# Optimization experiments

Hardware: AMD Instinct MI355X
Metric: run time of the kernel (lower is better)

The kernel has to match this reference:

```python
import jax, jax.numpy as jnp
import numpy as np

B, H, W = 64, 224, 224
EPS = 1e-5


def setup_inputs() -> dict:
    key = jax.random.key(0)
    ks = jax.random.split(key, 8)
    n = lambda k, s, std: jax.random.normal(k, s, jnp.float32) * std
    return {
        "x": jax.random.normal(ks[0], (B, 1, H, W), jnp.float32),
        "conv1_w": n(ks[1], (24, 1, 3, 3), 0.2),
        "conv1_b": jnp.zeros((24,), jnp.float32),
        "bn1_g": jnp.ones((24,), jnp.float32),
        "bn1_b": jnp.zeros((24,), jnp.float32),
        "conv2_w": n(ks[2], (48, 24, 3, 3), 0.07),
        "conv2_b": jnp.zeros((48,), jnp.float32),
        "bn2_g": jnp.ones((48,), jnp.float32),
        "bn2_b": jnp.zeros((48,), jnp.float32),
        "fconv_w": n(ks[3], (48, 48, 56, 56), 0.003),
        "fconv_b": jnp.zeros((48,), jnp.float32),
        "lin1_w": n(ks[4], (24, 48), 0.02),
        "lin1_b": jnp.zeros((24,), jnp.float32),
        "lin2_w": n(ks[5], (4, 24), 0.01),
        "lin2_b": jnp.array([0.0, 0.0, 1.0, 0.0], jnp.float32),  # torch init: identity transform bias
    }


def conv2d(x, w, b):
    y = jax.lax.conv_general_dilated(x, w, (1, 1), ((1, 1), (1, 1)),
                                     dimension_numbers=("NCHW", "OIHW", "NCHW"))
    return y + b[None, :, None, None]


def batchnorm(x, g, b):
    # train-mode BN: batch statistics over (N, H, W), biased variance
    m = x.mean((0, 2, 3), keepdims=True)
    v = x.var((0, 2, 3), keepdims=True)
    return (x - m) * jax.lax.rsqrt(v + EPS) * g[None, :, None, None] + b[None, :, None, None]


def maxpool2(x):
    b, c, h, w = x.shape
    return x.reshape(b, c, h // 2, 2, w // 2, 2).max(axis=(3, 5))


def affine_grid(theta, h, w):
    # theta: [B,2,3]; align_corners=False normalized coords (torch default)
    xs = (jnp.arange(w, dtype=jnp.float32) * 2 + 1) / w - 1.0
    ys = (jnp.arange(h, dtype=jnp.float32) * 2 + 1) / h - 1.0
    gx, gy = jnp.meshgrid(xs, ys)                      # [H,W] each
    base = jnp.stack([gx, gy, jnp.ones_like(gx)], -1)  # [H,W,3] (x, y, 1)
    return jnp.einsum("bij,hwj->bhwi", theta, base)    # [B,H,W,2] -> (x, y)


def grid_sample(img, grid):
    # bilinear, zeros padding, align_corners=False (torch defaults)
    b, c, h, w = img.shape
    ix = ((grid[..., 0] + 1.0) * w - 1.0) * 0.5        # [B,H,W]
    iy = ((grid[..., 1] + 1.0) * h - 1.0) * 0.5
    x0 = jnp.floor(ix); y0 = jnp.floor(iy)
    x1 = x0 + 1.0; y1 = y0 + 1.0
    wx1 = ix - x0; wx0 = 1.0 - wx1
    wy1 = iy - y0; wy0 = 1.0 - wy1
    bidx = jnp.arange(b)[:, None, None]

    def tap(xf, yf, wgt):
        valid = (xf >= 0) & (xf < w) & (yf >= 0) & (yf < h)
        xi = jnp.clip(xf, 0, w - 1).astype(jnp.int32)
        yi = jnp.clip(yf, 0, h - 1).astype(jnp.int32)
        vals = img[bidx, :, yi, xi]                    # [B,H,W,C]
        return vals * (wgt * valid)[..., None]

    out = (tap(x0, y0, wx0 * wy0) + tap(x1, y0, wx1 * wy0)
           + tap(x0, y1, wx0 * wy1) + tap(x1, y1, wx1 * wy1))
    return jnp.transpose(out, (0, 3, 1, 2))            # [B,C,H,W]


def reference(x, conv1_w, conv1_b, bn1_g, bn1_b, conv2_w, conv2_b, bn2_g, bn2_b,
              fconv_w, fconv_b, lin1_w, lin1_b, lin2_w, lin2_b):
    b, _, h, w = x.shape
    x1 = maxpool2(jax.nn.relu(batchnorm(conv2d(x, conv1_w, conv1_b), bn1_g, bn1_b)))
    x1 = maxpool2(jax.nn.relu(batchnorm(conv2d(x1, conv2_w, conv2_b), bn2_g, bn2_b)))
    # final_conv with kernel 56 over a 56x56 map == full contraction
    feat = jnp.einsum("bchw,ochw->bo", x1, fconv_w) + fconv_b      # [B,48]
    theta4 = jax.nn.relu(feat @ lin1_w.T + lin1_b) @ lin2_w.T + lin2_b  # [B,4]
    tx, ty, scale, angle = theta4[:, 0], theta4[:, 1], theta4[:, 2], theta4[:, 3]
    c, s = jnp.cos(angle), jnp.sin(angle)
    # (T @ R @ S)[:, :2] built directly, fully vectorized over batch
    row0 = jnp.stack([scale * c, -scale * s, tx], -1)
    row1 = jnp.stack([scale * s, scale * c, ty], -1)
    theta = jnp.stack([row0, row1], 1)                 # [B,2,3]
    grid = affine_grid(theta, h, w)
    out = grid_sample(x, grid)
    return out, tx, ty, scale, angle
```

## Files before the change

### kernel.cpp

```cpp
#include <hip/hip_runtime.h>
#include <hip/hip_bf16.h>

#define NB 64
#define H0 224
#define W0 224
#define C1 24
#define C2 48
#define H1 112
#define W1 112
#define H2 56
#define W2 56
#define EPSV 1e-5f

#define WS_STATS1   0
#define WS_STATS2   432
#define WS_FEAT     1296
#define WS_B2       4368
#define WS_X2       11280
#define WS_FWT      (WS_X2 + 4818944)
#define WS_X1       9645072
#define WS_NEED_BIG ((size_t)(WS_X1 + 9633792) * 4)
#define OUT0_ELEMS  (NB*H0*W0)

typedef _Float16 v8h __attribute__((ext_vector_type(8)));
typedef float    v4f __attribute__((ext_vector_type(4)));

static __device__ __forceinline__ unsigned short f2h(float v) {
    _Float16 h = (_Float16)v;
    unsigned short us;
    __builtin_memcpy(&us, &h, 2);
    return us;
}

__global__ __launch_bounds__(256) void k_init(const float* __restrict__ w2, float* __restrict__ ws)
{
    int t = blockIdx.x * 256 + threadIdx.x;
    if (t < WS_B2) ws[t] = 0.f;
    if (t < 13824) {
        int e = t & 7;
        int l = (t >> 3) & 63;
        int g = t >> 9;
        int q = l >> 4, ml = l & 15;
        int kp = g / 3, nt = g % 3;
        int ic = q * 8 + e;
        int oc = nt * 16 + ml;
        float v = (ic < C1) ? w2[(oc * C1 + ic) * 9 + kp] : 0.f;
        ((_Float16*)(ws + WS_B2))[t] = (_Float16)v;
    }
}

__global__ __launch_bounds__(256) void k_prep(const float* __restrict__ fw, _Float16* __restrict__ fwt)
{
    int t = blockIdx.x * 256 + threadIdx.x;
    if (t >= 903168) return;
    int o = t / 18816;
    int k = (t % 18816) * 8;
    const float* src = fw + (long)o * 150528 + k;
    float4 v0 = *(const float4*)src;
    float4 v1 = *(const float4*)(src + 4);
    uint4 u;
    u.x = (unsigned int)f2h(v0.x) | ((unsigned int)f2h(v0.y) << 16);
    u.y = (unsigned int)f2h(v0.z) | ((unsigned int)f2h(v0.w) << 16);
    u.z = (unsigned int)f2h(v1.x) | ((unsigned int)f2h(v1.y) << 16);
    u.w = (unsigned int)f2h(v1.z) | ((unsigned int)f2h(v1.w) << 16);
    int g = k >> 6, kin = k & 63;
    *(uint4*)&fwt[((long)(g * 48 + o)) * 64 + kin] = u;
}

__global__ __launch_bounds__(256) void k_conv1_pool_stats4(
    const float* __restrict__ x, const float* __restrict__ w1, const float* __restrict__ b1,
    float* __restrict__ ws, _Float16* __restrict__ x1g)
{
    __shared__ float xt[34][36];
    __shared__ unsigned int outt[256][13];
    __shared__ float sred[2 * C1];

    const int tid = threadIdx.x;
    const int b = blockIdx.z;
    const int py0 = blockIdx.y * 16, px0 = blockIdx.x * 16;
    const int iy0 = 2 * py0 - 1, ix0 = 2 * px0 - 1;
    const float* xb = x + b * (H0 * W0);

    for (int li = tid; li < 34 * 34; li += 256) {
        int ry = li / 34, rx = li % 34;
        int gy = iy0 + ry, gx = ix0 + rx;
        bool ok = (gy >= 0) & (gy < H0) & (gx >= 0) & (gx < W0);
        xt[ry][rx] = ok ? xb[gy * W0 + gx] : 0.f;
    }

    const int wid = tid >> 6;
    const int lane = tid & 63;
    const int c0 = wid * 6;

    const int c0s = __builtin_amdgcn_readfirstlane(c0);
    const float* __restrict__ wps = w1 + c0s * 9;
    float wr[54], br[6];
#pragma unroll
    for (int k = 0; k < 54; k++) wr[k] = wps[k];
#pragma unroll
    for (int c = 0; c < 6; c++) br[c] = b1[c0s + c];

    __syncthreads();

    float s[6] = {0.f, 0.f, 0.f, 0.f, 0.f, 0.f};
    float q[6] = {0.f, 0.f, 0.f, 0.f, 0.f, 0.f};
    const int pc = lane & 15;
    const int pr0 = lane >> 4;

#pragma unroll
    for (int pp = 0; pp < 4; pp++) {
        const int pr = pr0 + 4 * pp;
        float patch[16];
#pragma unroll
        for (int i2 = 0; i2 < 4; i2++)
#pragma unroll
            for (int j2 = 0; j2 < 4; j2++)
                patch[i2 * 4 + j2] = xt[2 * pr + i2][2 * pc + j2];

        unsigned int pk[3];
#pragma unroll
        for (int cp = 0; cp < 3; cp++) {
            unsigned int pv = 0;
#pragma unroll
            for (int h = 0; h < 2; h++) {
                int c = 2 * cp + h;
                float m4 = -1e30f;
#pragma unroll
                for (int sy = 0; sy < 2; sy++)
#pragma unroll
                    for (int sx = 0; sx < 2; sx++) {
                        float a = br[c];
#pragma unroll
                        for (int ky = 0; ky < 3; ky++)
#pragma unroll
                            for (int kx = 0; kx < 3; kx++)
                                a = fmaf(patch[(sy + ky) * 4 + (sx + kx)], wr[c * 9 + ky * 3 + kx], a);
                        s[c] += a;
                        q[c] = fmaf(a, a, q[c]);
                        m4 = fmaxf(m4, a);
                    }
                pv |= ((unsigned int)f2h(m4)) << (16 * h);
            }
            pk[cp] = pv;
        }
        int pos = pr * 16 + pc;
        outt[pos][wid * 3 + 0] = pk[0];
        outt[pos][wid * 3 + 1] = pk[1];
        outt[pos][wid * 3 + 2] = pk[2];
    }

#pragma unroll
    for (int c = 0; c < 6; c++) {
#pragma unroll
        for (int off = 32; off > 0; off >>= 1) {
            s[c] += __shfl_down(s[c], off, 64);
            q[c] += __shfl_down(q[c], off, 64);
        }
    }
    if (lane == 0) {
#pragma unroll
        for (int c = 0; c < 6; c++) {
            sred[c0 + c] = s[c];
            sred[C1 + c0 + c] = q[c];
        }
    }
    __syncthreads();

    if (tid < 2 * C1) {
        int cp = (blockIdx.x + 7 * blockIdx.y + 49 * blockIdx.z) & 7;
        atomicAdd(&ws[WS_STATS1 + cp * 2 * C1 + tid], sred[tid]);
    }

    for (int u = tid; u < 768; u += 256) {
        int pos = u / 3, prt = u % 3;
        int pr = pos >> 4, pcc = pos & 15;
        long p = (long)(b * H1 + (py0 + pr)) * W1 + (px0 + pcc);
        uint4 v;
        v.x = outt[pos][4 * prt + 0];
        v.y = outt[pos][4 * prt + 1];
        v.z = outt[pos][4 * prt + 2];
        v.w = outt[pos][4 * prt + 3];
        *(uint4*)(x1g + p * C1 + prt * 8) = v;
    }
}

__global__ __launch_bounds__(256, 2) void k_conv2_fused5(
    const _Float16* __restrict__ x1g, const _Float16* __restrict__ bpp,
    const float* __restrict__ g1, const float* __restrict__ bb1,
    const float* __restrict__ b2,
    float* __restrict__ ws, unsigned int* __restrict__ pooltu)
{
    __shared__ __align__(16) _Float16 x1t[2][10][18][32];
    __shared__ float alds[C1], bflds[C1];
    __shared__ float sred[2 * C2];

    const int tid = threadIdx.x;
    const int w = tid >> 6;
    const int lane = tid & 63;
    const int ml = lane & 15;
    const int qq = lane >> 4;

    v8h B[9][3];
#pragma unroll
    for (int kp = 0; kp < 9; kp++)
#pragma unroll
        for (int nt = 0; nt < 3; nt++)
            B[kp][nt] = *(const v8h*)&bpp[((kp * 3 + nt) * 64 + lane) * 8];

    if (tid < C1) {
        float s = 0.f, q = 0.f;
#pragma unroll
        for (int i = 0; i < 8; i++) {
            s += ws[WS_STATS1 + i * 2 * C1 + tid];
            q += ws[WS_STATS1 + i * 2 * C1 + C1 + tid];
        }
        const float N = (float)(NB * H0 * W0);
        float m = s / N;
        float v = q / N - m * m;
        float a = g1[tid] / sqrtf(v + EPSV);
        alds[tid] = a;
        bflds[tid] = bb1[tid] - m * a;
    }
    if (tid < 2 * C2) sred[tid] = 0.f;

    float bias[3] = {b2[ml], b2[16 + ml], b2[32 + ml]};

    int spart[3], spr[3], spc[3]; bool swrite[3];
#pragma unroll
    for (int it3 = 0; it3 < 3; it3++) {
        int li = tid + it3 * 256;
        swrite[it3] = li < 720;
        spart[it3] = li & 3;
        int pos = li >> 2;
        spr[it3] = pos / 18;
        spc[it3] = pos % 18;
    }

    const int nb = gridDim.x;
    const int NTILE = 6272;
    int qn = NTILE / nb, rn = NTILE % nb;
    int start = (blockIdx.x < rn) ? blockIdx.x * (qn + 1)
                                  : rn * (qn + 1) + (blockIdx.x - rn) * qn;
    int cnt = (blockIdx.x < rn) ? qn + 1 : qn;

    float svacc[3] = {0.f, 0.f, 0.f}, qvacc[3] = {0.f, 0.f, 0.f};

    v8h raw[3];
    bool inb_n[3];
    {
        int t = start;
        int tb = t / 98, rem = t % 98;
        int ty = (rem / 7) * 8, txx = (rem % 7) * 16;
#pragma unroll
        for (int it3 = 0; it3 < 3; it3++) {
#pragma unroll
            for (int e = 0; e < 8; e++) raw[it3][e] = (_Float16)0.f;
            int gy = ty - 1 + spr[it3], gx = txx - 1 + spc[it3];
            inb_n[it3] = swrite[it3] & (spart[it3] < 3) &
                         (gy >= 0) & (gy < H1) & (gx >= 0) & (gx < W1);
            if (inb_n[it3])
                raw[it3] = *(const v8h*)&x1g[((tb * H1 + gy) * W1 + gx) * C1 + spart[it3] * 8];
        }
    }
    __syncthreads();

#pragma unroll
    for (int it3 = 0; it3 < 3; it3++) {
        if (swrite[it3]) {
            v8h r8;
            if (inb_n[it3]) {
#pragma unroll
                for (int e = 0; e < 8; e++) {
                    int c = spart[it3] * 8 + e;
                    float vv = fmaxf(fmaf((float)raw[it3][e], alds[c], bflds[c]), 0.f);
                    r8[e] = (_Float16)vv;
                }
            } else {
#pragma unroll
                for (int e = 0; e < 8; e++) r8[e] = (_Float16)0.f;
            }
            *(v8h*)&x1t[0][spr[it3]][spc[it3]][spart[it3] * 8] = r8;
        }
    }
    __syncthreads();

    for (int it = 0; it < cnt; it++) {
        const int cur = it & 1;
        const int t = start + it;
        const int tb = t / 98, rem = t % 98;
        const int ty = (rem / 7) * 8, txx = (rem % 7) * 16;

        const bool haveNext = (it + 1 < cnt);
        if (haveNext) {
            int t2 = t + 1;
            int nb2 = t2 / 98, rem2 = t2 % 98;
            int ny = (rem2 / 7) * 8, nx = (rem2 % 7) * 16;
#pragma unroll
            for (int it3 = 0; it3 < 3; it3++) {
#pragma unroll
                for (int e = 0; e < 8; e++) raw[it3][e] = (_Float16)0.f;
                int gy = ny - 1 + spr[it3], gx = nx - 1 + spc[it3];
                inb_n[it3] = swrite[it3] & (spart[it3] < 3) &
                             (gy >= 0) & (gy < H1) & (gx >= 0) & (gx < W1);
                if (inb_n[it3])
                    raw[it3] = *(const v8h*)&x1g[((nb2 * H1 + gy) * W1 + gx) * C1 + spart[it3] * 8];
            }
        }

        v4f acc[2][3];
#pragma unroll
        for (int mt = 0; mt < 2; mt++)
#pragma unroll
            for (int nt = 0; nt < 3; nt++)
                acc[mt][nt] = (v4f){0.f, 0.f, 0.f, 0.f};

#pragma unroll
        for (int kp = 0; kp < 9; kp++) {
            const int ky = kp / 3, kx = kp % 3;
#pragma unroll
            for (int mt = 0; mt < 2; mt++) {
                const int r = 2 * w + mt;
                v8h a = *(const v8h*)&x1t[cur][r + ky][ml + kx][qq * 8];
                acc[mt][0] = __builtin_amdgcn_mfma_f32_16x16x32_f16(a, B[kp][0], acc[mt][0], 0, 0, 0);
                acc[mt][1] = __builtin_amdgcn_mfma_f32_16x16x32_f16(a, B[kp][1], acc[mt][1], 0, 0, 0);
                acc[mt][2] = __builtin_amdgcn_mfma_f32_16x16x32_f16(a, B[kp][2], acc[mt][2], 0, 0, 0);
            }
        }

#pragma unroll
        for (int nt = 0; nt < 3; nt++) {
            int oc = nt * 16 + ml;
            float z[2][4];
#pragma unroll
            for (int mt = 0; mt < 2; mt++)
#pragma unroll
                for (int rg = 0; rg < 4; rg++) {
                    float val = acc[mt][nt][rg] + bias[nt];
                    z[mt][rg] = val;
                    svacc[nt] += val;
                    qvacc[nt] = fmaf(val, val, qvacc[nt]);
                }
            int py = (ty >> 1) + w;
            float m0 = fmaxf(fmaxf(z[0][0], z[0][1]), fmaxf(z[1][0], z[1][1]));
            float m1 = fmaxf(fmaxf(z[0][2], z[0][3]), fmaxf(z[1][2], z[1][3]));
            int px0 = (txx >> 1) + qq * 2;
            int k = oc * 3136 + py * W2 + px0;
            unsigned int pk2 = (unsigned int)f2h(m0) | ((unsigned int)f2h(m1) << 16);
            pooltu[(((k >> 6) * NB + tb) << 5) + ((k & 63) >> 1)] = pk2;
        }

        if (haveNext) {
#pragma unroll
            for (int it3 = 0; it3 < 3; it3++) {
                if (swrite[it3]) {
                    v8h r8;
                    if (inb_n[it3]) {
#pragma unroll
                        for (int e = 0; e < 8; e++) {
                            int c = spart[it3] * 8 + e;
                            float vv = fmaxf(fmaf((float)raw[it3][e], alds[c], bflds[c]), 0.f);
                            r8[e] = (_Float16)vv;
                        }
                    } else {
#pragma unroll
                        for (int e = 0; e < 8; e++) r8[e] = (_Float16)0.f;
                    }
                    *(v8h*)&x1t[cur ^ 1][spr[it3]][spc[it3]][spart[it3] * 8] = r8;
                }
            }
        }
        __syncthreads();
    }

#pragma unroll
    for (int nt = 0; nt < 3; nt++) {
        float sv = svacc[nt], qv = qvacc[nt];
        sv += __shfl_xor(sv, 16, 64); qv += __shfl_xor(qv, 16, 64);
        sv += __shfl_xor(sv, 32, 64); qv += __shfl_xor(qv, 32, 64);
        if (qq == 0) {
            atomicAdd(&sred[nt * 16 + ml], sv);
            atomicAdd(&sred[C2 + nt * 16 + ml], qv);
        }
    }
    __syncthreads();
    if (tid < 2 * C2) {
        atomicAdd(&ws[WS_STATS2 + (blockIdx.x & 7) * 2 * C2 + tid], sred[tid]);
    }
}

__global__ __launch_bounds__(256) void k_fconv5(
    const unsigned int* __restrict__ pooltu, const _Float16* __restrict__ fwt,
    const float* __restrict__ ws, const float* __restrict__ g2, const float* __restrict__ bb2,
    float* __restrict__ part)
{
    __shared__ __align__(16) _Float16 fwh[48][136];
    __shared__ __align__(16) _Float16 x2h[64][136];
    __shared__ float csh[2 * C2];

    const int tid = threadIdx.x;
    const int bx = blockIdx.x;

    const uint4* fsrc = (const uint4*)fwt + (long)bx * 768;
    const uint4* psrc = (const uint4*)pooltu + (long)bx * 1024;
    uint4 fr[3], pr[4];
#pragma unroll
    for (int t3 = 0; t3 < 3; t3++) fr[t3] = fsrc[tid + 256 * t3];
#pragma unroll
    for (int t4 = 0; t4 < 4; t4++) pr[t4] = psrc[tid + 256 * t4];

    if (tid < C2) {
        int c = tid;
        float s = 0.f, q = 0.f;
#pragma unroll
        for (int i = 0; i < 8; i++) {
            s += ws[WS_STATS2 + i * 2 * C2 + c];
            q += ws[WS_STATS2 + i * 2 * C2 + C2 + c];
        }
        const float N = (float)(NB * H1 * W1);
        float m = s / N;
        float v = q / N - m * m;
        float a = g2[c] / sqrtf(v + EPSV);
        csh[c] = a;
        csh[C2 + c] = bb2[c] - m * a;
    }
    __syncthreads();

#pragma unroll
    for (int t3 = 0; t3 < 3; t3++) {
        int li = tid + 256 * t3;
        int gg = li / 384;
        int o = (li % 384) / 8;
        int kin = (li & 7) * 8;
        *(uint4*)&fwh[o][gg * 64 + kin] = fr[t3];
    }
    const int c0 = (2 * bx) / 49, c1 = (2 * bx + 1) / 49;
    const float a0 = csh[c0], bf0 = csh[C2 + c0];
    const float a1 = csh[c1], bf1 = csh[C2 + c1];
#pragma unroll
    for (int t4 = 0; t4 < 4; t4++) {
        int li = tid + 256 * t4;
        int gg = li >> 9;
        int b = (li & 511) >> 3;
        int kin = (li & 7) * 8;
        float aa = gg ? a1 : a0;
        float bb = gg ? bf1 : bf0;
        union { uint4 u; v8h h; } cv;
        cv.u = pr[t4];
        v8h r8;
#pragma unroll
        for (int e = 0; e < 8; e++)
            r8[e] = (_Float16)fmaxf(fmaf((float)cv.h[e], aa, bb), 0.f);
        *(v8h*)&x2h[b][gg * 64 + kin] = r8;
    }
    __syncthreads();

    const int w = tid >> 6;
    const int lane = tid & 63;
    const int ml = lane & 15;
    const int qq = lane >> 4;

    v4f acc[3];
#pragma unroll
    for (int ot = 0; ot < 3; ot++) acc[ot] = (v4f){0.f, 0.f, 0.f, 0.f};

#pragma unroll
    for (int ks = 0; ks < 4; ks++) {
        v8h a = *(const v8h*)&x2h[w * 16 + ml][ks * 32 + qq * 8];
#pragma unroll
        for (int ot = 0; ot < 3; ot++) {
            v8h bb = *(const v8h*)&fwh[ot * 16 + ml][ks * 32 + qq * 8];
            acc[ot] = __builtin_amdgcn_mfma_f32_16x16x32_f16(a, bb, acc[ot], 0, 0, 0);
        }
    }

    float* po = part + (long)bx * (NB * C2);
#pragma unroll
    for (int ot = 0; ot < 3; ot++)
#pragma unroll
        for (int rg = 0; rg < 4; rg++)
            po[(w * 16 + qq * 4 + rg) * C2 + ot * 16 + ml] = acc[ot][rg];
}

__global__ __launch_bounds__(256) void k_freduce3(const float* __restrict__ part, float* __restrict__ feat)
{
    const int t = (blockIdx.x % 12) * 256 + threadIdx.x;
    const int seg = blockIdx.x / 12;
    float s = 0.f;
    for (int bl = seg * 147; bl < (seg + 1) * 147; bl++)
        s += part[(long)bl * (NB * C2) + t];
    atomicAdd(&feat[t], s);
}

__global__ __launch_bounds__(64) void k_theta2(
    const float* __restrict__ feat, const float* __restrict__ fcb,
    const float* __restrict__ l1w, const float* __restrict__ l1b,
    const float* __restrict__ l2w, const float* __restrict__ l2b,
    float* __restrict__ tmat, float* __restrict__ out)
{
    const int b = threadIdx.x;
    float f[C2];
#pragma unroll
    for (int o = 0; o < C2; o++) f[o] = feat[b * C2 + o] + fcb[o];
    float h[24];
#pragma unroll
    for (int jj = 0; jj < 24; jj++) {
        float a = l1b[jj];
#pragma unroll
        for (int o = 0; o < C2; o++) a = fmaf(f[o], l1w[jj * C2 + o], a);
        h[jj] = fmaxf(a, 0.f);
    }
    float th[4];
#pragma unroll
    for (int k = 0; k < 4; k++) {
        float a = l2b[k];
#pragma unroll
        for (int jj = 0; jj < 24; jj++) a = fmaf(h[jj], l2w[k * 24 + jj], a);
        th[k] = a;
        out[OUT0_ELEMS + k * NB + b] = a;
    }
    float sc = th[2], an = th[3];
    float cc = cosf(an), ss = sinf(an);
    tmat[0 * NB + b] = sc * cc;
    tmat[1 * NB + b] = -sc * ss;
    tmat[2 * NB + b] = sc * ss;
    tmat[3 * NB + b] = sc * cc;
    tmat[4 * NB + b] = th[0];
    tmat[5 * NB + b] = th[1];
}

__global__ __launch_bounds__(256) void k_sample3(
    const float* __restrict__ x, const float* __restrict__ tmat, float* __restrict__ out)
{
    const int b = blockIdx.y;
    const float t00 = tmat[0 * NB + b], t01 = tmat[1 * NB + b];
    const float t10 = tmat[2 * NB + b], t11 = tmat[3 * NB + b];
    const float tx  = tmat[4 * NB + b], ty  = tmat[5 * NB + b];
    const float* xb = x + b * (H0 * W0);

    int idx = (blockIdx.x * 256 + threadIdx.x) * 2;
    int i = idx / W0, j = idx % W0;
    float ys = (2.f * (float)i + 1.f) / (float)H0 - 1.f;

    float o2[2];
#pragma unroll
    for (int px = 0; px < 2; px++) {
        float xs = (2.f * (float)(j + px) + 1.f) / (float)W0 - 1.f;
        float gx = t00 * xs + t01 * ys + tx;
        float gy = t10 * xs + t11 * ys + ty;
        float ix = ((gx + 1.f) * (float)W0 - 1.f) * 0.5f;
        float iy = ((gy + 1.f) * (float)H0 - 1.f) * 0.5f;
        float x0 = floorf(ix), y0 = floorf(iy);
        float x1f = x0 + 1.f, y1f = y0 + 1.f;
        float wx1 = ix - x0, wx0 = 1.f - wx1;
        float wy1 = iy - y0, wy0 = 1.f - wy1;
        auto tap = [&](float xf, float yf, float wgt) -> float {
            bool valid = (xf >= 0.f) & (xf < (float)W0) & (yf >= 0.f) & (yf < (float)H0);
            int xi = (int)fminf(fmaxf(xf, 0.f), (float)(W0 - 1));
            int yi = (int)fminf(fmaxf(yf, 0.f), (float)(H0 - 1));
            return valid ? xb[yi * W0 + xi] * wgt : 0.f;
        };
        o2[px] = tap(x0, y0, wx0 * wy0) + tap(x1f, y0, wx1 * wy0)
               + tap(x0, y1f, wx0 * wy1) + tap(x1f, y1f, wx1 * wy1);
    }
    *(float2*)&out[(b * H0 + i) * W0 + j] = make_float2(o2[0], o2[1]);
}

__global__ __launch_bounds__(256) void k_conv1_stats(
    const float* __restrict__ x, const float* __restrict__ w1, const float* __restrict__ b1,
    float* __restrict__ ws)
{
    float s[C1], q[C1];
#pragma unroll
    for (int c = 0; c < C1; c++) { s[c] = 0.f; q[c] = 0.f; }
    const int NT = gridDim.x * 256;
    const int total = NB * H0 * W0;
    for (int p = blockIdx.x * 256 + threadIdx.x; p < total; p += NT) {
        int b = p / (H0 * W0);
        int r = p % (H0 * W0);
        int y = r / W0;
        int xx = r % W0;
        const float* xb = x + b * (H0 * W0);
        float patch[9];
#pragma unroll
        for (int dy = 0; dy < 3; dy++)
#pragma unroll
            for (int dx = 0; dx < 3; dx++) {
                int yy = y + dy - 1, xc = xx + dx - 1;
                bool ok = (yy >= 0) & (yy < H0) & (xc >= 0) & (xc < W0);
                patch[dy * 3 + dx] = ok ? xb[yy * W0 + xc] : 0.f;
            }
#pragma unroll
        for (int c = 0; c < C1; c++) {
            const float* wp = w1 + c * 9;
            float a = b1[c];
#pragma unroll
            for (int k = 0; k < 9; k++) a = fmaf(patch[k], wp[k], a);
            s[c] += a;
            q[c] = fmaf(a, a, q[c]);
        }
    }
#pragma unroll
    for (int c = 0; c < C1; c++) {
#pragma unroll
        for (int off = 32; off > 0; off >>= 1) {
            s[c] += __shfl_down(s[c], off, 64);
            q[c] += __shfl_down(q[c], off, 64);
        }
    }
    __shared__ float sred[2 * C1];
    if (threadIdx.x < 2 * C1) sred[threadIdx.x] = 0.f;
    __syncthreads();
    if ((threadIdx.x & 63) == 0) {
#pragma unroll
        for (int c = 0; c < C1; c++) {
            atomicAdd(&sred[c], s[c]);
            atomicAdd(&sred[C1 + c], q[c]);
        }
    }
    __syncthreads();
    if (threadIdx.x < 2 * C1) {
        atomicAdd(&ws[WS_STATS1 + (blockIdx.x & 7) * 2 * C1 + threadIdx.x], sred[threadIdx.x]);
    }
}

__global__ __launch_bounds__(256, 2) void k_conv2_fused(
    const float* __restrict__ x, const float* __restrict__ w1, const float* __restrict__ b1,
    const float* __restrict__ g1, const float* __restrict__ bb1,
    const _Float16* __restrict__ bpp, const float* __restrict__ b2,
    float* __restrict__ ws, float* __restrict__ pool)
{
    __shared__ float xt[22][38];
    __shared__ __align__(16) _Float16 x1t[10][18][32];
    __shared__ __align__(16) _Float16 Blds[13824];
    __shared__ float wlds[C1 * 9];
    __shared__ float blds[C1], alds[C1], bflds[C1];
    __shared__ float sred[2 * C2];

    const int tid = threadIdx.x;
    const int b = blockIdx.z;
    const int y0 = blockIdx.y * 8;
    const int x0 = blockIdx.x * 16;
    const float* xb = x + b * (H0 * W0);

    for (int li = tid; li < 13824 / 8; li += 256)
        ((uint4*)Blds)[li] = ((const uint4*)bpp)[li];

    if (tid < C1 * 9) wlds[tid] = w1[tid];
    if (tid < C1) {
        float s = 0.f, q = 0.f;
#pragma unroll
        for (int i = 0; i < 8; i++) {
            s += ws[WS_STATS1 + i * 2 * C1 + tid];
            q += ws[WS_STATS1 + i * 2 * C1 + C1 + tid];
        }
        const float N = (float)(NB * H0 * W0);
        float m = s / N;
        float v = q / N - m * m;
        float a = g1[tid] / sqrtf(v + EPSV);
        blds[tid] = b1[tid];
        alds[tid] = a;
        bflds[tid] = bb1[tid] - m * a;
    }
    if (tid < 2 * C2) sred[tid] = 0.f;

    const int oy0 = 2 * y0 - 3, ox0 = 2 * x0 - 3;
    for (int li = tid; li < 22 * 38; li += 256) {
        int ry = li / 38, rx = li % 38;
        int gy = oy0 + ry, gx = ox0 + rx;
        bool ok = (gy >= 0) & (gy < H0) & (gx >= 0) & (gx < W0);
        xt[ry][rx] = ok ? xb[gy * W0 + gx] : 0.f;
    }
    __syncthreads();

    if (tid < 180) {
        int pr = tid / 18, pc = tid % 18;
        int gy = y0 - 1 + pr, gx = x0 - 1 + pc;
        bool valid = (gy >= 0) & (gy < H1) & (gx >= 0) & (gx < W1);
        float patch[16];
#pragma unroll
        for (int dy = 0; dy < 4; dy++)
#pragma unroll
            for (int dx = 0; dx < 4; dx++)
                patch[dy * 4 + dx] = xt[2 * pr + dy][2 * pc + dx];
        unsigned int* dst = (unsigned int*)&x1t[pr][pc][0];
#pragma unroll
        for (int cp = 0; cp < 12; cp++) {
            unsigned int pk = 0;
#pragma unroll
            for (int h = 0; h < 2; h++) {
                int c = 2 * cp + h;
                float m4 = -1e30f;
#pragma unroll
                for (int py = 0; py < 2; py++)
#pragma unroll
                    for (int px = 0; px < 2; px++) {
                        float a = blds[c];
#pragma unroll
                        for (int ky = 0; ky < 3; ky++)
#pragma unroll
                            for (int kx = 0; kx < 3; kx++)
                                a = fmaf(patch[(py + ky) * 4 + (px + kx)], wlds[c * 9 + ky * 3 + kx], a);
                        m4 = fmaxf(m4, fmaf(a, alds[c], bflds[c]));
                    }
                float v = valid ? fmaxf(m4, 0.f) : 0.f;
                pk |= ((unsigned int)f2h(v)) << (16 * h);
            }
            dst[cp] = pk;
        }
        dst[12] = 0; dst[13] = 0; dst[14] = 0; dst[15] = 0;
    }
    __syncthreads();

    const int w = tid >> 6;
    const int lane = tid & 63;
    const int ml = lane & 15;
    const int q = lane >> 4;

    v4f acc[2][3];
#pragma unroll
    for (int mt = 0; mt < 2; mt++)
#pragma unroll
        for (int nt = 0; nt < 3; nt++)
            acc[mt][nt] = (v4f){0.f, 0.f, 0.f, 0.f};

#pragma unroll
    for (int kp = 0; kp < 9; kp++) {
        const int ky = kp / 3, kx = kp % 3;
        v8h B0 = *(const v8h*)&Blds[((kp * 3 + 0) * 64 + lane) * 8];
        v8h B1 = *(const v8h*)&Blds[((kp * 3 + 1) * 64 + lane) * 8];
        v8h B2 = *(const v8h*)&Blds[((kp * 3 + 2) * 64 + lane) * 8];
#pragma unroll
        for (int mt = 0; mt < 2; mt++) {
            const int r = 2 * w + mt;
            v8h a = *(const v8h*)&x1t[r + ky][ml + kx][q * 8];
            acc[mt][0] = __builtin_amdgcn_mfma_f32_16x16x32_f16(a, B0, acc[mt][0], 0, 0, 0);
            acc[mt][1] = __builtin_amdgcn_mfma_f32_16x16x32_f16(a, B1, acc[mt][1], 0, 0, 0);
            acc[mt][2] = __builtin_amdgcn_mfma_f32_16x16x32_f16(a, B2, acc[mt][2], 0, 0, 0);
        }
    }

#pragma unroll
    for (int nt = 0; nt < 3; nt++) {
        int oc = nt * 16 + ml;
        float bias = b2[oc];
        float z[2][4];
        float sv = 0.f, qv = 0.f;
#pragma unroll
        for (int mt = 0; mt < 2; mt++)
#pragma unroll
            for (int rg = 0; rg < 4; rg++) {
                float val = acc[mt][nt][rg] + bias;
                z[mt][rg] = val;
                sv += val;
                qv = fmaf(val, val, qv);
            }
        sv += __shfl_xor(sv, 16, 64); qv += __shfl_xor(qv, 16, 64);
        sv += __shfl_xor(sv, 32, 64); qv += __shfl_xor(qv, 32, 64);
        if (q == 0) { atomicAdd(&sred[oc], sv); atomicAdd(&sred[C2 + oc], qv); }

        int py = (y0 >> 1) + w;
#pragma unroll
        for (int j = 0; j < 2; j++) {
            float m = fmaxf(fmaxf(z[0][2 * j], z[0][2 * j + 1]),
                            fmaxf(z[1][2 * j], z[1][2 * j + 1]));
            int px = (x0 >> 1) + q * 2 + j;
            pool[((b * C2 + oc) * H2 + py) * W2 + px] = m;
        }
    }
    __syncthreads();
    if (tid < 2 * C2) {
        int cp = (blockIdx.x + 7 * blockIdx.y + 31 * blockIdx.z) & 7;
        atomicAdd(&ws[WS_STATS2 + cp * 2 * C2 + tid], sred[tid]);
    }
}

#define KC 512
#define KSUB 128
__global__ __launch_bounds__(256) void k_fconv(
    const float* __restrict__ pool, const float* __restrict__ ws,
    const float* __restrict__ g2, const float* __restrict__ bb2,
    const float* __restrict__ fw, float* __restrict__ feat)
{
    __shared__ float fwt[C2][KSUB + 1];
    __shared__ float x2t[NB][KSUB + 1];
    __shared__ float csh[2 * C2];
    if (threadIdx.x < C2) {
        int c = threadIdx.x;
        float s = 0.f, q = 0.f;
#pragma unroll
        for (int i = 0; i < 8; i++) {
            s += ws[WS_STATS2 + i * 2 * C2 + c];
            q += ws[WS_STATS2 + i * 2 * C2 + C2 + c];
        }
        const float N = (float)(NB * H1 * W1);
        float m = s / N;
        float v = q / N - m * m;
        float a = g2[c] / sqrtf(v + EPSV);
        csh[c] = a;
        csh[C2 + c] = bb2[c] - m * a;
    }
    int k0 = blockIdx.x * KC;
    int i = threadIdx.x / 16, j = threadIdx.x % 16;
    float acc[3][4] = {{0.f}};
    for (int sub = 0; sub < KC / KSUB; sub++) {
        int kb = k0 + sub * KSUB;
        __syncthreads();
        for (int li = threadIdx.x; li < C2 * KSUB; li += 256) {
            int o = li / KSUB, k = li % KSUB;
            fwt[o][k] = fw[o * 150528 + kb + k];
        }
        for (int li = threadIdx.x; li < NB * KSUB; li += 256) {
            int b = li / KSUB, k = li % KSUB;
            int kk = kb + k;
            int c = kk / (H2 * W2);
            float v = pool[b * 150528 + kk];
            x2t[b][k] = fmaxf(fmaf(v, csh[c], csh[C2 + c]), 0.f);
        }
        __syncthreads();
        for (int k = 0; k < KSUB; k++) {
            float fa[3], xv[4];
#pragma unroll
            for (int c = 0; c < 3; c++) fa[c] = fwt[i + 16 * c][k];
#pragma unroll
            for (int d = 0; d < 4; d++) xv[d] = x2t[j + 16 * d][k];
#pragma unroll
            for (int c = 0; c < 3; c++)
#pragma unroll
                for (int d = 0; d < 4; d++)
                    acc[c][d] = fmaf(fa[c], xv[d], acc[c][d]);
        }
    }
#pragma unroll
    for (int c = 0; c < 3; c++)
#pragma unroll
        for (int d = 0; d < 4; d++)
            atomicAdd(&feat[(j + 16 * d) * C2 + (i + 16 * c)], acc[c][d]);
}

__global__ __launch_bounds__(256) void k_sample(
    const float* __restrict__ x, const float* __restrict__ feat, const float* __restrict__ fcb,
    const float* __restrict__ l1w, const float* __restrict__ l1b,
    const float* __restrict__ l2w, const float* __restrict__ l2b,
    float* __restrict__ out)
{
    __shared__ float hsh[24];
    __shared__ float th[4];
    int b = blockIdx.y;
    int tid = threadIdx.x;
    if (tid < 24) {
        float a = l1b[tid];
        for (int o = 0; o < C2; o++)
            a = fmaf(feat[b * C2 + o] + fcb[o], l1w[tid * C2 + o], a);
        hsh[tid] = fmaxf(a, 0.f);
    }
    __syncthreads();
    if (tid < 4) {
        float a = l2b[tid];
        for (int jj = 0; jj < 24; jj++) a = fmaf(hsh[jj], l2w[tid * 24 + jj], a);
        th[tid] = a;
        if (blockIdx.x == 0) out[OUT0_ELEMS + tid * NB + b] = a;
    }
    __syncthreads();

    int idx = blockIdx.x * 256 + tid;
    int i = idx / W0, j = idx % W0;
    float tx = th[0], ty = th[1], sc = th[2], an = th[3];
    float cc = cosf(an), ss = sinf(an);
    float t00 = sc * cc, t01 = -sc * ss, t10 = sc * ss, t11 = sc * cc;
    float xs = (2.f * (float)j + 1.f) / (float)W0 - 1.f;
    float ys = (2.f * (float)i + 1.f) / (float)H0 - 1.f;
    float gx = t00 * xs + t01 * ys + tx;
    float gy = t10 * xs + t11 * ys + ty;
    float ix = ((gx + 1.f) * (float)W0 - 1.f) * 0.5f;
    float iy = ((gy + 1.f) * (float)H0 - 1.f) * 0.5f;
    float x0 = floorf(ix), y0 = floorf(iy);
    float x1f = x0 + 1.f, y1f = y0 + 1.f;
    float wx1 = ix - x0, wx0 = 1.f - wx1;
    float wy1 = iy - y0, wy0 = 1.f - wy1;
    const float* xb = x + b * (H0 * W0);
    auto tap = [&](float xf, float yf, float wgt) -> float {
        bool valid = (xf >= 0.f) & (xf < (float)W0) & (yf >= 0.f) & (yf < (float)H0);
        int xi = (int)fminf(fmaxf(xf, 0.f), (float)(W0 - 1));
        int yi = (int)fminf(fmaxf(yf, 0.f), (float)(H0 - 1));
        return valid ? xb[yi * W0 + xi] * wgt : 0.f;
    };
    float o = tap(x0, y0, wx0 * wy0) + tap(x1f, y0, wx1 * wy0)
            + tap(x0, y1f, wx0 * wy1) + tap(x1f, y1f, wx1 * wy1);
    out[(b * H0 + i) * W0 + j] = o;
}

extern "C" void kernel_launch(void* const* d_in, const int* in_sizes, int n_in,
                              void* d_out, int out_size, void* d_ws, size_t ws_size,
                              hipStream_t stream)
{
    const float* x    = (const float*)d_in[0];
    const float* c1w  = (const float*)d_in[1];
    const float* c1b  = (const float*)d_in[2];
    const float* bn1g = (const float*)d_in[3];
    const float* bn1b = (const float*)d_in[4];
    const float* c2w  = (const float*)d_in[5];
    const float* c2b  = (const float*)d_in[6];
    const float* bn2g = (const float*)d_in[7];
    const float* bn2b = (const float*)d_in[8];
    const float* fw   = (const float*)d_in[9];
    const float* fcb  = (const float*)d_in[10];
    const float* l1w  = (const float*)d_in[11];
    const float* l1b  = (const float*)d_in[12];
    const float* l2w  = (const float*)d_in[13];
    const float* l2b  = (const float*)d_in[14];
    float* ws  = (float*)d_ws;
    float* out = (float*)d_out;

    k_init<<<dim3(54), 256, 0, stream>>>(c2w, ws);

    if (ws_size >= WS_NEED_BIG) {
        k_prep<<<dim3(3528), 256, 0, stream>>>(fw, (_Float16*)(ws + WS_FWT));
        k_conv1_pool_stats4<<<dim3(7, 7, 64), 256, 0, stream>>>(
            x, c1w, c1b, ws, (_Float16*)(ws + WS_X1));
        k_conv2_fused5<<<dim3(512), 256, 0, stream>>>(
            (const _Float16*)(ws + WS_X1), (const _Float16*)(ws + WS_B2),
            bn1g, bn1b, c2b, ws, (unsigned int*)(ws + WS_X2));
        k_fconv5<<<dim3(1176), 256, 0, stream>>>(
            (const unsigned int*)(ws + WS_X2), (const _Float16*)(ws + WS_FWT),
            ws, bn2g, bn2b, ws + WS_X1);
        k_freduce3<<<dim3(96), 256, 0, stream>>>(ws + WS_X1, ws + WS_FEAT);
        k_theta2<<<dim3(1), 64, 0, stream>>>(
            ws + WS_FEAT, fcb, l1w, l1b, l2w, l2b, ws + WS_B2, out);
        k_sample3<<<dim3(98, 64), 256, 0, stream>>>(x, ws + WS_B2, out);
    } else {
        k_conv1_stats<<<dim3(1024), 256, 0, stream>>>(x, c1w, c1b, ws);
        k_conv2_fused<<<dim3(7, 14, 64), 256, 0, stream>>>(
            x, c1w, c1b, bn1g, bn1b, (const _Float16*)(ws + WS_B2), c2b, ws, ws + WS_X2);
        k_fconv<<<dim3(150528 / KC), 256, 0, stream>>>(ws + WS_X2, ws, bn2g, bn2b, fw, ws + WS_FEAT);
        k_sample<<<dim3(196, 64), 256, 0, stream>>>(x, ws + WS_FEAT, fcb, l1w, l1b, l2w, l2b, out);
    }
}
```

Baseline: 248.6 us.

## Merge init with weight prep via LDS transpose; replace partial reduce with atomics

Folds the workspace init into a new weight-prep kernel. That kernel stages a 48x512 slab of fconv weights in shared memory and writes the fp16 blocked layout with coalesced 16-byte stores, cutting block count from 3528 to 294. The fconv kernel now atomically adds its MFMA accumulators straight into the feature buffer, dropping the partial-sum buffer and the separate reduce kernel. This removes two launches and a large partial write/read, at the cost of heavy atomic contention (1176 blocks onto 3072 addresses) and order-dependent float summation.

```diff
diff --git a/kernel.cpp b/kernel.cpp
--- a/kernel.cpp
+++ b/kernel.cpp
@@ -32,39 +32,52 @@
     return us;
 }
 
-__global__ __launch_bounds__(256) void k_init(const float* __restrict__ w2, float* __restrict__ ws)
-{
-    int t = blockIdx.x * 256 + threadIdx.x;
-    if (t < WS_B2) ws[t] = 0.f;
-    if (t < 13824) {
-        int e = t & 7;
-        int l = (t >> 3) & 63;
-        int g = t >> 9;
-        int q = l >> 4, ml = l & 15;
-        int kp = g / 3, nt = g % 3;
-        int ic = q * 8 + e;
-        int oc = nt * 16 + ml;
-        float v = (ic < C1) ? w2[(oc * C1 + ic) * 9 + kp] : 0.f;
-        ((_Float16*)(ws + WS_B2))[t] = (_Float16)v;
-    }
-}
-
-__global__ __launch_bounds__(256) void k_prep(const float* __restrict__ fw, _Float16* __restrict__ fwt)
-{
-    int t = blockIdx.x * 256 + threadIdx.x;
-    if (t >= 903168) return;
-    int o = t / 18816;
-    int k = (t % 18816) * 8;
-    const float* src = fw + (long)o * 150528 + k;
-    float4 v0 = *(const float4*)src;
-    float4 v1 = *(const float4*)(src + 4);
-    uint4 u;
-    u.x = (unsigned int)f2h(v0.x) | ((unsigned int)f2h(v0.y) << 16);
-    u.y = (unsigned int)f2h(v0.z) | ((unsigned int)f2h(v0.w) << 16);
-    u.z = (unsigned int)f2h(v1.x) | ((unsigned int)f2h(v1.y) << 16);
-    u.w = (unsigned int)f2h(v1.z) | ((unsigned int)f2h(v1.w) << 16);
-    int g = k >> 6, kin = k & 63;
-    *(uint4*)&fwt[((long)(g * 48 + o)) * 64 + kin] = u;
+__global__ __launch_bounds__(256) void k_initprep(
+    const float* __restrict__ w2, const float* __restrict__ fw,
+    float* __restrict__ ws, _Float16* __restrict__ fwt)
+{
+    __shared__ _Float16 T[48][520];
+    const int tid = threadIdx.x;
+    const int bx = blockIdx.x;
+
+    if (bx < 54) {
+        int t = bx * 256 + tid;
+        if (t < WS_B2) ws[t] = 0.f;
+        if (t < 13824) {
+            int e = t & 7;
+            int l = (t >> 3) & 63;
+            int g = t >> 9;
+            int q = l >> 4, ml = l & 15;
+            int kp = g / 3, nt = g % 3;
+            int ic = q * 8 + e;
+            int oc = nt * 16 + ml;
+            float v = (ic < C1) ? w2[(oc * C1 + ic) * 9 + kp] : 0.f;
+            ((_Float16*)(ws + WS_B2))[t] = (_Float16)v;
+        }
+    }
+
+    const int kb = bx * 512;
+#pragma unroll
+    for (int t3 = 0; t3 < 24; t3++) {
+        int li = tid + 256 * t3;
+        int o = li / 128, k4 = li % 128;
+        float4 v = *(const float4*)&fw[(long)o * 150528 + kb + 4 * k4];
+        T[o][4 * k4 + 0] = (_Float16)v.x;
+        T[o][4 * k4 + 1] = (_Float16)v.y;
+        T[o][4 * k4 + 2] = (_Float16)v.z;
+        T[o][4 * k4 + 3] = (_Float16)v.w;
+    }
+    __syncthreads();
+    uint4* dst = (uint4*)&fwt[(long)kb * 48];
+#pragma unroll
+    for (int t3 = 0; t3 < 12; t3++) {
+        int u = tid + 256 * t3;
+        int gg = u / 384;
+        int rem = u % 384;
+        int o = rem / 8;
+        int k8 = (rem % 8) * 8;
+        dst[u] = *(const uint4*)&T[o][gg * 64 + k8];
+    }
 }
 
 __global__ __launch_bounds__(256) void k_conv1_pool_stats4(
@@ -388,10 +401,10 @@
     }
 }
 
-__global__ __launch_bounds__(256) void k_fconv5(
+__global__ __launch_bounds__(256) void k_fconv6(
     const unsigned int* __restrict__ pooltu, const _Float16* __restrict__ fwt,
     const float* __restrict__ ws, const float* __restrict__ g2, const float* __restrict__ bb2,
-    float* __restrict__ part)
+    float* __restrict__ feat)
 {
     __shared__ __align__(16) _Float16 fwh[48][136];
     __shared__ __align__(16) _Float16 x2h[64][136];
@@ -473,22 +486,11 @@
         }
     }
 
-    float* po = part + (long)bx * (NB * C2);
 #pragma unroll
     for (int ot = 0; ot < 3; ot++)
 #pragma unroll
         for (int rg = 0; rg < 4; rg++)
-            po[(w * 16 + qq * 4 + rg) * C2 + ot * 16 + ml] = acc[ot][rg];
-}
-
-__global__ __launch_bounds__(256) void k_freduce3(const float* __restrict__ part, float* __restrict__ feat)
-{
-    const int t = (blockIdx.x % 12) * 256 + threadIdx.x;
-    const int seg = blockIdx.x / 12;
-    float s = 0.f;
-    for (int bl = seg * 147; bl < (seg + 1) * 147; bl++)
-        s += part[(long)bl * (NB * C2) + t];
-    atomicAdd(&feat[t], s);
+            atomicAdd(&feat[(w * 16 + qq * 4 + rg) * C2 + ot * 16 + ml], acc[ot][rg]);
 }
 
 __global__ __launch_bounds__(64) void k_theta2(
@@ -563,6 +565,23 @@
                + tap(x0, y1f, wx0 * wy1) + tap(x1f, y1f, wx1 * wy1);
     }
     *(float2*)&out[(b * H0 + i) * W0 + j] = make_float2(o2[0], o2[1]);
+}
+
+__global__ __launch_bounds__(256) void k_init(const float* __restrict__ w2, float* __restrict__ ws)
+{
+    int t = blockIdx.x * 256 + threadIdx.x;
+    if (t < WS_B2) ws[t] = 0.f;
+    if (t < 13824) {
+        int e = t & 7;
+        int l = (t >> 3) & 63;
+        int g = t >> 9;
+        int q = l >> 4, ml = l & 15;
+        int kp = g / 3, nt = g % 3;
+        int ic = q * 8 + e;
+        int oc = nt * 16 + ml;
+        float v = (ic < C1) ? w2[(oc * C1 + ic) * 9 + kp] : 0.f;
+        ((_Float16*)(ws + WS_B2))[t] = (_Float16)v;
+    }
 }
 
 __global__ __launch_bounds__(256) void k_conv1_stats(
@@ -911,23 +930,21 @@
     float* ws  = (float*)d_ws;
     float* out = (float*)d_out;
 
-    k_init<<<dim3(54), 256, 0, stream>>>(c2w, ws);
-
     if (ws_size >= WS_NEED_BIG) {
-        k_prep<<<dim3(3528), 256, 0, stream>>>(fw, (_Float16*)(ws + WS_FWT));
+        k_initprep<<<dim3(294), 256, 0, stream>>>(c2w, fw, ws, (_Float16*)(ws + WS_FWT));
         k_conv1_pool_stats4<<<dim3(7, 7, 64), 256, 0, stream>>>(
             x, c1w, c1b, ws, (_Float16*)(ws + WS_X1));
         k_conv2_fused5<<<dim3(512), 256, 0, stream>>>(
             (const _Float16*)(ws + WS_X1), (const _Float16*)(ws + WS_B2),
             bn1g, bn1b, c2b, ws, (unsigned int*)(ws + WS_X2));
-        k_fconv5<<<dim3(1176), 256, 0, stream>>>(
+        k_fconv6<<<dim3(1176), 256, 0, stream>>>(
             (const unsigned int*)(ws + WS_X2), (const _Float16*)(ws + WS_FWT),
-            ws, bn2g, bn2b, ws + WS_X1);
-        k_freduce3<<<dim3(96), 256, 0, stream>>>(ws + WS_X1, ws + WS_FEAT);
+            ws, bn2g, bn2b, ws + WS_FEAT);
         k_theta2<<<dim3(1), 64, 0, stream>>>(
             ws + WS_FEAT, fcb, l1w, l1b, l2w, l2b, ws + WS_B2, out);
         k_sample3<<<dim3(98, 64), 256, 0, stream>>>(x, ws + WS_B2, out);
     } else {
+        k_init<<<dim3(54), 256, 0, stream>>>(c2w, ws);
         k_conv1_stats<<<dim3(1024), 256, 0, stream>>>(x, c1w, c1b, ws);
         k_conv2_fused<<<dim3(7, 14, 64), 256, 0, stream>>>(
             x, c1w, c1b, bn1g, bn1b, (const _Float16*)(ws + WS_B2), c2b, ws, ws + WS_X2);
```

New measurement: 247.5 us. Within noise of the previous version (-0.5%).
